# Optimization experiments

Hardware: AMD Instinct MI355X
Metric: run time of the kernel (lower is better)

Reference implementation:

```python
import jax, jax.numpy as jnp
import numpy as np

DIM = 33  # hardcoded in the torch module


def setup_inputs() -> dict:
    key = jax.random.key(0)
    k1, k2, k3 = jax.random.split(key, 3)
    B, H, W = 8, 512, 512
    inp = jax.random.uniform(k1, (B, 3, H, W), dtype=jnp.float32)
    out = jax.random.uniform(k2, (B, 3, H, W), dtype=jnp.float32)
    mask = (jax.random.uniform(k3, (B, 1, H, W)) > 0.5).astype(jnp.float32)
    return {"mask": mask, "input": inp, "output": out}


def _tridistribute(mask, inp, out, dim=DIM):
    # Trilinear scatter-accumulate of `out` pixel colors into a per-image
    # 3D LUT indexed by `inp` pixel colors, masked, then count-normalized.
    B = inp.shape[0]
    binsize = 1.000001 / (dim - 1)
    x = inp / binsize                              # [B,3,H,W]
    idx = jnp.floor(x).astype(jnp.int32)           # lower bin ids, in [0, dim-2]
    frac = x - jnp.floor(x)                        # trilinear fractions
    r_id, g_id, b_id = idx[:, 0], idx[:, 1], idx[:, 2]
    rd = frac[:, 0].reshape(B, -1)                 # [B,N], N = H*W
    gd = frac[:, 1].reshape(B, -1)
    bd = frac[:, 2].reshape(B, -1)
    base = (r_id + g_id * dim + b_id * dim * dim).reshape(B, -1)  # flat corner 000
    m = (mask[:, 0] > 0).astype(inp.dtype).reshape(B, -1)
    ws, offs = [], []
    for db in (0, 1):
        for dg in (0, 1):
            for dr in (0, 1):
                w = ((rd if dr else 1 - rd) * (gd if dg else 1 - gd) * (bd if db else 1 - bd))
                ws.append(w * m)
                offs.append(dr + dg * dim + db * dim * dim)
    w_all = jnp.stack(ws, 0)                                        # [8,B,N]
    idx_all = base[None] + jnp.asarray(offs, jnp.int32)[:, None, None]  # [8,B,N]
    idx_flat = idx_all.transpose(1, 0, 2).reshape(B, -1)            # [B,8N]
    w_flat = w_all.transpose(1, 0, 2).reshape(B, -1)                # [B,8N]
    out_f = out.reshape(B, 3, -1)                                   # [B,3,N]
    vals = (w_all[:, :, None, :] * out_f[None]).transpose(1, 2, 0, 3).reshape(B, 3, -1)  # [B,3,8N]
    nbins = dim ** 3
    # scatter-add per batch element (vmap over B, then over 3 channels)
    lut = jax.vmap(lambda i, v: jax.vmap(lambda vc: jnp.zeros(nbins, inp.dtype).at[i].add(vc))(v))(idx_flat, vals)  # [B,3,nbins]
    cnt1 = jax.vmap(lambda i, w: jnp.zeros(nbins, inp.dtype).at[i].add(w))(idx_flat, w_flat)  # [B,nbins]
    cnt = jnp.broadcast_to(cnt1[:, None, :], lut.shape)             # same count for all 3 channels
    denom = jnp.where(cnt > 0, cnt, 1.0)
    lut = jnp.where(cnt > 0, lut / denom, 0.0)                      # tridistribute.divide
    shape5 = (B, 3, dim, dim, dim)
    return lut.reshape(shape5), cnt.reshape(shape5)


def reference(mask, input, output):
    lut, lut_count = _tridistribute(mask, input, output)
    return lut, lut_count, output
```

## Files before the change

### kernel.cpp

```cpp
#include <hip/hip_runtime.h>
#include <hip/hip_fp16.h>

#define DIM   33
#define NB    (DIM * DIM * DIM)
#define BATCH 8
#define HW    (512 * 512)
#define SLICE (DIM * DIM)
#define NK1   32
#define CAP1  4416
#define W1    256
#define SPAN1 1024
#define SUB2  4
#define NKEY  1024
#define CAP2  192
#define MAXC2 1120

#define G1_OFF 0
#define G2_OFF 256
#define NCNT   (G2_OFF + BATCH * NKEY)
#define A1     8448
#define S1     (BATCH * NK1 * CAP1)
#define A2     (A1 + 3 * S1)
#define S2     (BATCH * NKEY * CAP2)
#define WS_WORDS (A2 + 3 * S2)

static __device__ __forceinline__ unsigned f2h(float x) {
    return (unsigned)__half_as_ushort(__float2half(x));
}
static __device__ __forceinline__ float h2f(unsigned u) {
    return __half2float(__ushort_as_half((unsigned short)(u & 0xffffu)));
}
static __device__ __forceinline__ unsigned pack2(float a, float b) {
    return f2h(a) | (f2h(b) << 16);
}

__global__ __launch_bounds__(256) void zero_counters(int* __restrict__ ws)
{
    int i = blockIdx.x * 256 + threadIdx.x;
    if (i < NCNT) ws[i] = 0;
}

__global__ __launch_bounds__(256) void sort1(const float* __restrict__ mask,
                                             const float* __restrict__ inp,
                                             const float* __restrict__ outp,
                                             int* __restrict__ ws,
                                             float* __restrict__ outcopy)
{
    __shared__ int hist[NK1], basev[NK1], startL[NK1];
    __shared__ unsigned       stX[SPAN1];
    __shared__ unsigned       stY[SPAN1];
    __shared__ unsigned       o01[SPAN1];
    __shared__ unsigned short o2h[SPAN1];
    __shared__ unsigned short rnk[SPAN1];
    __shared__ unsigned short sidx[SPAN1];

    const int bid = blockIdx.x;
    const int w   = bid & (W1 - 1);
    const int b   = bid >> 8;

    if (threadIdx.x < NK1) hist[threadIdx.x] = 0;
    __syncthreads();

    const float binsize = 1.000001f / 32.0f;
    const size_t off = (size_t)w * SPAN1;
    const float* mk  = mask + (size_t)b * HW + off;
    const float* inR = inp  + (size_t)b * 3 * HW + off;
    const float* inG = inR + HW;
    const float* inB = inR + 2 * HW;
    const float* oR  = outp + (size_t)b * 3 * HW + off;
    const float* oG  = oR + HW;
    const float* oB  = oR + 2 * HW;
    float* cR = outcopy + (size_t)b * 3 * HW + off;
    float* cG = cR + HW;
    float* cB = cR + 2 * HW;

    const int o = threadIdx.x * 4;

    {
        float4 mv = *(const float4*)(mk + o);
        float4 rv = *(const float4*)(inR + o);
        float4 gv = *(const float4*)(inG + o);
        float4 bv = *(const float4*)(inB + o);
        float4 a0 = *(const float4*)(oR + o);
        float4 a1 = *(const float4*)(oG + o);
        float4 a2 = *(const float4*)(oB + o);

        *(float4*)(cR + o) = a0;
        *(float4*)(cG + o) = a1;
        *(float4*)(cB + o) = a2;

        float mm[4] = {mv.x, mv.y, mv.z, mv.w};
        float rr[4] = {rv.x, rv.y, rv.z, rv.w};
        float gg[4] = {gv.x, gv.y, gv.z, gv.w};
        float bb[4] = {bv.x, bv.y, bv.z, bv.w};
        float q0[4] = {a0.x, a0.y, a0.z, a0.w};
        float q1[4] = {a1.x, a1.y, a1.z, a1.w};
        float q2[4] = {a2.x, a2.y, a2.z, a2.w};
        #pragma unroll
        for (int r = 0; r < 4; ++r) {
            o01[o + r] = pack2(q0[r], q1[r]);
            o2h[o + r] = (unsigned short)f2h(q2[r]);
            unsigned sx = 0, sy = 0;
            if (mm[r] > 0.0f) {
                float xr = rr[r] / binsize;
                float xg = gg[r] / binsize;
                float xb = bb[r] / binsize;
                float fr = floorf(xr), fg = floorf(xg), fb = floorf(xb);
                int ir = (int)fr, ig = (int)fg, ib = (int)fb;
                int rd12 = (int)((xr - fr) * 4095.0f + 0.5f);
                int gd12 = (int)((xg - fg) * 4095.0f + 0.5f);
                int bd12 = (int)((xb - fb) * 4095.0f + 0.5f);
                sx = (unsigned)ir | ((unsigned)ig << 5) | ((unsigned)rd12 << 10)
                   | ((unsigned)(gd12 & 0x3FF) << 22);
                sy = (unsigned)(gd12 >> 10) | ((unsigned)bd12 << 2)
                   | ((unsigned)ib << 14) | (1u << 19);
                rnk[o + r] = (unsigned short)atomicAdd(&hist[ib], 1);
            }
            stX[o + r] = sx;
            stY[o + r] = sy;
        }
    }
    __syncthreads();

    if (threadIdx.x < NK1) {
        int c = hist[threadIdx.x];
        basev[threadIdx.x] = c ? atomicAdd(&ws[G1_OFF + b * NK1 + threadIdx.x], c) : 0;
        int v = c;
        #pragma unroll
        for (int d = 1; d < 32; d <<= 1) {
            int t = __shfl_up(v, d);
            if (threadIdx.x >= d) v += t;
        }
        startL[threadIdx.x] = v - c;
    }
    __syncthreads();

    {
        #pragma unroll
        for (int r = 0; r < 4; ++r) {
            unsigned sy = stY[o + r];
            if (sy >> 19) {
                int k = (sy >> 14) & 31;
                sidx[startL[k] + rnk[o + r]] = (unsigned short)(o + r);
            }
        }
    }
    __syncthreads();

    const int nlive = startL[NK1 - 1] + hist[NK1 - 1];
    unsigned* x1 = (unsigned*)(ws + A1);
    unsigned* y1 = x1 + S1;
    unsigned* z1 = x1 + 2 * S1;
    for (int j = threadIdx.x; j < nlive; j += 256) {
        int t = sidx[j];
        unsigned sy = stY[t];
        int k = (sy >> 14) & 31;
        int gs = basev[k] + (j - startL[k]);
        if (gs < CAP1) {
            size_t base = (size_t)(b * NK1 + k) * CAP1 + gs;
            x1[base] = stX[t];
            y1[base] = (sy & 0x3FFFu) | ((o01[t] & 0xFFFFu) << 14);
            z1[base] = (o01[t] >> 16) | ((unsigned)o2h[t] << 16);
        }
    }
}

__global__ __launch_bounds__(256) void sort2(int* __restrict__ ws)
{
    __shared__ unsigned       xL[MAXC2], yL[MAXC2], zL[MAXC2];
    __shared__ unsigned short rnkL[MAXC2], sidxL[MAXC2];
    __shared__ int hist[32], basev[32], startL[32];

    const int bid = blockIdx.x;
    const int s   = bid & (SUB2 - 1);
    const int ib  = (bid >> 2) & 31;
    const int b   = bid >> 7;

    if (threadIdx.x < 32) hist[threadIdx.x] = 0;
    __syncthreads();

    int n1 = ws[G1_OFF + b * NK1 + ib];
    if (n1 > CAP1) n1 = CAP1;
    const int beg = n1 * s / SUB2;
    const int end = n1 * (s + 1) / SUB2;
    const int cntn = end - beg;

    const unsigned* x1 = (const unsigned*)(ws + A1);
    const unsigned* y1 = x1 + S1;
    const unsigned* z1 = x1 + 2 * S1;
    const size_t base1 = (size_t)(b * NK1 + ib) * CAP1 + beg;

    for (int i = threadIdx.x; i < cntn; i += 256) {
        unsigned x = x1[base1 + i];
        xL[i] = x;
        yL[i] = y1[base1 + i];
        zL[i] = z1[base1 + i];
        rnkL[i] = (unsigned short)atomicAdd(&hist[(x >> 5) & 31], 1);
    }
    __syncthreads();

    if (threadIdx.x < 32) {
        int c = hist[threadIdx.x];
        basev[threadIdx.x] = c
            ? atomicAdd(&ws[G2_OFF + ((b << 10) | (threadIdx.x << 5) | ib)], c) : 0;
        int v = c;
        #pragma unroll
        for (int d = 1; d < 32; d <<= 1) {
            int t = __shfl_up(v, d);
            if (threadIdx.x >= d) v += t;
        }
        startL[threadIdx.x] = v - c;
    }
    __syncthreads();

    for (int i = threadIdx.x; i < cntn; i += 256) {
        int k = (xL[i] >> 5) & 31;
        sidxL[startL[k] + rnkL[i]] = (unsigned short)i;
    }
    __syncthreads();

    unsigned* x2 = (unsigned*)(ws + A2);
    unsigned* y2 = x2 + S2;
    unsigned* z2 = x2 + 2 * S2;
    for (int j = threadIdx.x; j < cntn; j += 256) {
        int t = sidxL[j];
        unsigned x = xL[t];
        int k = (x >> 5) & 31;
        int gs = basev[k] + (j - startL[k]);
        if (gs < CAP2) {
            size_t b2 = (size_t)((b << 10) | (k << 5) | ib) * CAP2 + gs;
            x2[b2] = x;
            y2[b2] = yL[t];
            z2[b2] = zL[t];
        }
    }
}

__global__ __launch_bounds__(256) void gather_pass(const int* __restrict__ ws,
                                                   float* __restrict__ lut,
                                                   float* __restrict__ cnt)
{
    __shared__ float4 vL[4][CAP2];
    __shared__ float  rdL[4][CAP2];
    __shared__ int    histL[4][32];
    __shared__ int    startL[4][32];
    __shared__ float  partL[4][64][4];

    const int bid   = blockIdx.x;
    const int b     = bid / SLICE;
    const int rem   = bid % SLICE;
    const int gOut  = rem / DIM;
    const int blOut = rem % DIM;

    const int wv    = threadIdx.x >> 6;
    const int lane  = threadIdx.x & 63;
    const int ghalf = (wv >> 1) & 1;
    const int bhalf = wv & 1;
    const int ig    = gOut - 1 + ghalf;
    const int ib    = blOut - 1 + bhalf;
    const bool valid = ((unsigned)ig < 32u) && ((unsigned)ib < 32u);

    if (lane < 32) histL[wv][lane] = 0;
    __syncthreads();

    const unsigned* x2 = (const unsigned*)(ws + A2);
    const unsigned* y2 = x2 + S2;
    const unsigned* z2 = x2 + 2 * S2;

    const float inv = 1.0f / 4095.0f;
    int n = 0;
    int    ranks[3] = {0, 0, 0};
    int    irs[3]   = {0, 0, 0};
    float4 vreg[3];
    float  rdreg[3] = {0.f, 0.f, 0.f};
    if (valid) {
        int key = (ig << 5) | ib;
        n = ws[G2_OFF + ((b << 10) | key)];
        if (n > CAP2) n = CAP2;
        size_t kb = (size_t)((b << 10) | key) * CAP2;
        #pragma unroll
        for (int t = 0; t < 3; ++t) {
            int i = lane + t * 64;
            if (i < n) {
                unsigned x = x2[kb + i];
                unsigned y = y2[kb + i];
                unsigned z = z2[kb + i];
                float rd = (float)((x >> 10) & 0xFFF) * inv;
                float gd = (float)(((x >> 22) & 0x3FF) | ((y & 3u) << 10)) * inv;
                float bd = (float)((y >> 2) & 0xFFF) * inv;
                float o0 = h2f(y >> 14);
                float o1 = h2f(z);
                float o2 = h2f(z >> 16);
                float wg_ = ghalf ? (1.0f - gd) : gd;
                float wb_ = bhalf ? (1.0f - bd) : bd;
                float wgb = wg_ * wb_;
                vreg[t]  = make_float4(wgb * o0, wgb * o1, wgb * o2, wgb);
                rdreg[t] = rd;
                irs[t]   = x & 31;
                ranks[t] = atomicAdd(&histL[wv][irs[t]], 1);
            }
        }
    }
    __syncthreads();

    {
        int h = (lane < 32) ? histL[wv][lane] : 0;
        int v = h;
        #pragma unroll
        for (int o = 1; o < 32; o <<= 1) {
            int t = __shfl_up(v, o, 32);
            if ((lane & 31) >= o) v += t;
        }
        if (lane < 32) startL[wv][lane] = v - h;
    }
    __syncthreads();

    if (valid) {
        #pragma unroll
        for (int t = 0; t < 3; ++t) {
            int i = lane + t * 64;
            if (i < n) {
                int pos = startL[wv][irs[t]] + ranks[t];
                vL[wv][pos]  = vreg[t];
                rdL[wv][pos] = rdreg[t];
            }
        }
    }
    __syncthreads();

    float4 acc = make_float4(0.f, 0.f, 0.f, 0.f);
    if (valid) {
        const int run = lane >> 1;
        const int kk  = lane & 1;
        int s = startL[wv][run];
        int e = s + histL[wv][run];
        for (int j = s; j < e; ++j) {
            float4 v = vL[wv][j];
            float rd = rdL[wv][j];
            float wr_ = kk ? (1.0f - rd) : rd;
            acc.x += wr_ * v.x;
            acc.y += wr_ * v.y;
            acc.z += wr_ * v.z;
            acc.w += wr_ * v.w;
        }
    }
    *(float4*)partL[wv][lane] = acc;
    __syncthreads();

    if (threadIdx.x < DIM * 4) {
        int r  = threadIdx.x >> 2;
        int ch = threadIdx.x & 3;
        float v = 0.f, c = 0.f;
        #pragma unroll
        for (int w2 = 0; w2 < 4; ++w2) {
            if (r < 32) {
                v += partL[w2][2 * r + 1][ch == 3 ? 3 : ch];
                c += partL[w2][2 * r + 1][3];
            }
            if (r > 0) {
                v += partL[w2][2 * r - 2][ch == 3 ? 3 : ch];
                c += partL[w2][2 * r - 2][3];
            }
        }
        int bin = r + gOut * DIM + blOut * SLICE;
        size_t ob = (size_t)b * 3 * NB;
        if (ch == 3) {
            cnt[ob + bin]          = c;
            cnt[ob + NB + bin]     = c;
            cnt[ob + 2 * NB + bin] = c;
        } else {
            lut[ob + (size_t)ch * NB + bin] = (c > 0.0f) ? v / c : 0.0f;
        }
    }
}

__global__ void tridist_scatter(const float* __restrict__ mask,
                                const float* __restrict__ inp,
                                const float* __restrict__ outp,
                                float* __restrict__ lut,
                                float* __restrict__ cnt)
{
    int i = blockIdx.x * blockDim.x + threadIdx.x;
    if (i >= BATCH * HW) return;
    int b = i / HW;
    int p = i - b * HW;

    float m = mask[(size_t)b * HW + p];
    if (!(m > 0.0f)) return;

    const float binsize = 1.000001f / 32.0f;
    size_t ibase = (size_t)b * 3 * HW + p;
    float xr = inp[ibase] / binsize;
    float xg = inp[ibase + HW] / binsize;
    float xb = inp[ibase + 2 * HW] / binsize;
    float flr = floorf(xr), flg = floorf(xg), flb = floorf(xb);
    int ir = (int)flr, ig = (int)flg, ib = (int)flb;
    float rd = xr - flr, gd = xg - flg, bd = xb - flb;
    int base = ir + ig * DIM + ib * DIM * DIM;
    float o0 = outp[ibase], o1 = outp[ibase + HW], o2 = outp[ibase + 2 * HW];
    float wr[2] = {1.0f - rd, rd};
    float wg_[2] = {1.0f - gd, gd};
    float wb[2] = {1.0f - bd, bd};
    float* lut0 = lut + (size_t)b * 3 * NB;
    float* cnt0 = cnt + (size_t)b * 3 * NB;
    #pragma unroll
    for (int db = 0; db < 2; ++db)
        #pragma unroll
        for (int dg = 0; dg < 2; ++dg)
            #pragma unroll
            for (int dr = 0; dr < 2; ++dr) {
                float wv2 = (wr[dr] * wg_[dg]) * wb[db];
                int bin = base + dr + dg * DIM + db * DIM * DIM;
                atomicAdd(cnt0 + bin, wv2);
                atomicAdd(lut0 + bin, wv2 * o0);
                atomicAdd(lut0 + NB + bin, wv2 * o1);
                atomicAdd(lut0 + 2 * NB + bin, wv2 * o2);
            }
}

__global__ void tridist_finalize(float* __restrict__ lut, float* __restrict__ cnt)
{
    int i = blockIdx.x * blockDim.x + threadIdx.x;
    if (i >= BATCH * NB) return;
    int b = i / NB;
    int j = i - b * NB;
    float c = cnt[(size_t)b * 3 * NB + j];
    bool nz = (c > 0.0f);
    #pragma unroll
    for (int ch = 0; ch < 3; ++ch) {
        size_t off = ((size_t)b * 3 + ch) * NB + j;
        float v = lut[off];
        lut[off] = nz ? (v / c) : 0.0f;
        cnt[off] = c;
    }
}

__global__ void copy_out(const float4* __restrict__ src,
                         float4* __restrict__ dst, int n4)
{
    int i = blockIdx.x * blockDim.x + threadIdx.x;
    int stride = gridDim.x * blockDim.x;
    for (; i < n4; i += stride) dst[i] = src[i];
}

extern "C" void kernel_launch(void* const* d_in, const int* in_sizes, int n_in,
                              void* d_out, int out_size, void* d_ws, size_t ws_size,
                              hipStream_t stream)
{
    const float* mask = (const float*)d_in[0];
    const float* inp  = (const float*)d_in[1];
    const float* outp = (const float*)d_in[2];

    float* out     = (float*)d_out;
    float* lut     = out;
    float* cnt     = out + (size_t)BATCH * 3 * NB;
    float* outcopy = out + (size_t)2 * BATCH * 3 * NB;

    size_t need = (size_t)WS_WORDS * sizeof(int);

    if (ws_size >= need) {
        int* ws = (int*)d_ws;
        zero_counters<<<(NCNT + 255) / 256, 256, 0, stream>>>(ws);
        sort1<<<BATCH * W1, 256, 0, stream>>>(mask, inp, outp, ws, outcopy);
        sort2<<<BATCH * NK1 * SUB2, 256, 0, stream>>>(ws);
        gather_pass<<<BATCH * SLICE, 256, 0, stream>>>(ws, lut, cnt);
    } else {
        hipMemsetAsync(out, 0, (size_t)2 * BATCH * 3 * NB * sizeof(float), stream);
        tridist_scatter<<<(BATCH * HW + 255) / 256, 256, 0, stream>>>(mask, inp, outp, lut, cnt);
        tridist_finalize<<<(BATCH * NB + 255) / 256, 256, 0, stream>>>(lut, cnt);
        int n4 = BATCH * 3 * HW / 4;
        copy_out<<<2048, 256, 0, stream>>>((const float4*)outp, (float4*)outcopy, n4);
    }
}
```

Baseline: 63.01 us.

## Sort by joint g/r key in sort2 and pass run tables to gather

sort2 now builds a 1024-bin joint histogram over (g-bin, r-bin), so each bucket it writes out is already ordered by r within each of its four sub-chunks. It also writes a per-key run-offset table (absRun) into the workspace. gather_pass reads these offsets directly and drops its shared-memory histogram, atomics, scan and scatter, along with two of its barriers. In exchange, sort2 does a larger 1024-entry scan, extra table writes and extra global reads in gather, and each lane now loops over four segments instead of one.

```diff
diff --git a/kernel.cpp b/kernel.cpp
--- a/kernel.cpp
+++ b/kernel.cpp
@@ -22,7 +22,9 @@
 #define S1     (BATCH * NK1 * CAP1)
 #define A2     (A1 + 3 * S1)
 #define S2     (BATCH * NKEY * CAP2)
-#define WS_WORDS (A2 + 3 * S2)
+#define RT_OFF (A2 + 3 * S2)
+#define RT_ENT (BATCH * NKEY * SUB2 * 33)
+#define WS_WORDS (RT_OFF + (RT_ENT + 1) / 2)
 
 static __device__ __forceinline__ unsigned f2h(float x) {
     return (unsigned)__half_as_ushort(__float2half(x));
@@ -165,18 +167,24 @@
     }
 }
 
-__global__ __launch_bounds__(256) void sort2(int* __restrict__ ws)
+__global__ __launch_bounds__(256) void sort2(int* __restrict__ ws,
+                                             unsigned short* __restrict__ absRun)
 {
     __shared__ unsigned       xL[MAXC2], yL[MAXC2], zL[MAXC2];
     __shared__ unsigned short rnkL[MAXC2], sidxL[MAXC2];
-    __shared__ int hist[32], basev[32], startL[32];
+    __shared__ int hist[1024];
+    __shared__ int startL[1024];
+    __shared__ int basev[32];
+    __shared__ int wsum[4];
 
     const int bid = blockIdx.x;
     const int s   = bid & (SUB2 - 1);
     const int ib  = (bid >> 2) & 31;
     const int b   = bid >> 7;
-
-    if (threadIdx.x < 32) hist[threadIdx.x] = 0;
+    const int tid = threadIdx.x;
+
+    #pragma unroll
+    for (int k = 0; k < 4; ++k) hist[tid + k * 256] = 0;
     __syncthreads();
 
     int n1 = ws[G1_OFF + b * NK1 + ib];
@@ -190,60 +198,93 @@
     const unsigned* z1 = x1 + 2 * S1;
     const size_t base1 = (size_t)(b * NK1 + ib) * CAP1 + beg;
 
-    for (int i = threadIdx.x; i < cntn; i += 256) {
+    for (int i = tid; i < cntn; i += 256) {
         unsigned x = x1[base1 + i];
         xL[i] = x;
         yL[i] = y1[base1 + i];
         zL[i] = z1[base1 + i];
-        rnkL[i] = (unsigned short)atomicAdd(&hist[(x >> 5) & 31], 1);
-    }
-    __syncthreads();
-
-    if (threadIdx.x < 32) {
-        int c = hist[threadIdx.x];
-        basev[threadIdx.x] = c
-            ? atomicAdd(&ws[G2_OFF + ((b << 10) | (threadIdx.x << 5) | ib)], c) : 0;
-        int v = c;
-        #pragma unroll
-        for (int d = 1; d < 32; d <<= 1) {
+        int joint = (((x >> 5) & 31) << 5) | (x & 31);
+        rnkL[i] = (unsigned short)atomicAdd(&hist[joint], 1);
+    }
+    __syncthreads();
+
+    int sums[4];
+    int local = 0;
+    {
+        const int b4 = tid * 4;
+        #pragma unroll
+        for (int k = 0; k < 4; ++k) { sums[k] = local; local += hist[b4 + k]; }
+        int lane = tid & 63, wid = tid >> 6;
+        int v = local;
+        #pragma unroll
+        for (int d = 1; d < 64; d <<= 1) {
             int t = __shfl_up(v, d);
-            if (threadIdx.x >= d) v += t;
-        }
-        startL[threadIdx.x] = v - c;
-    }
-    __syncthreads();
-
-    for (int i = threadIdx.x; i < cntn; i += 256) {
-        int k = (xL[i] >> 5) & 31;
-        sidxL[startL[k] + rnkL[i]] = (unsigned short)i;
+            if (lane >= d) v += t;
+        }
+        if (lane == 63) wsum[wid] = v;
+        __syncthreads();
+        if (tid == 0) {
+            int a = 0;
+            #pragma unroll
+            for (int w2 = 0; w2 < 4; ++w2) { int t = wsum[w2]; wsum[w2] = a; a += t; }
+        }
+        __syncthreads();
+        int excl = v - local + wsum[wid];
+        const int b4b = tid * 4;
+        #pragma unroll
+        for (int k = 0; k < 4; ++k) startL[b4b + k] = excl + sums[k];
+    }
+    __syncthreads();
+
+    if (tid < 32) {
+        int keyStart = startL[tid << 5];
+        int keyEnd   = (tid == 31) ? cntn : startL[(tid + 1) << 5];
+        int c = keyEnd - keyStart;
+        basev[tid] = c
+            ? atomicAdd(&ws[G2_OFF + ((b << 10) | (tid << 5) | ib)], c) : 0;
+    }
+    __syncthreads();
+
+    for (int i = tid; i < cntn; i += 256) {
+        unsigned x = xL[i];
+        int joint = (((x >> 5) & 31) << 5) | (x & 31);
+        sidxL[startL[joint] + rnkL[i]] = (unsigned short)i;
+    }
+    for (int e = tid; e < 32 * 33; e += 256) {
+        int ig = e / 33, r = e - ig * 33;
+        int keyStart = startL[ig << 5];
+        int keyEnd   = (ig == 31) ? cntn : startL[(ig + 1) << 5];
+        int rel = (r == 32) ? (keyEnd - keyStart)
+                            : (startL[(ig << 5) + r] - keyStart);
+        size_t idx = ((size_t)((b << 10) | (ig << 5) | ib) * SUB2 + s) * 33 + r;
+        absRun[idx] = (unsigned short)(basev[ig] + rel);
     }
     __syncthreads();
 
     unsigned* x2 = (unsigned*)(ws + A2);
     unsigned* y2 = x2 + S2;
     unsigned* z2 = x2 + 2 * S2;
-    for (int j = threadIdx.x; j < cntn; j += 256) {
+    for (int j = tid; j < cntn; j += 256) {
         int t = sidxL[j];
         unsigned x = xL[t];
-        int k = (x >> 5) & 31;
-        int gs = basev[k] + (j - startL[k]);
+        int ig = (x >> 5) & 31;
+        int gs = basev[ig] + (j - startL[ig << 5]);
         if (gs < CAP2) {
-            size_t b2 = (size_t)((b << 10) | (k << 5) | ib) * CAP2 + gs;
-            x2[b2] = x;
-            y2[b2] = yL[t];
-            z2[b2] = zL[t];
+            size_t d = (size_t)((b << 10) | (ig << 5) | ib) * CAP2 + gs;
+            x2[d] = x;
+            y2[d] = yL[t];
+            z2[d] = zL[t];
         }
     }
 }
 
 __global__ __launch_bounds__(256) void gather_pass(const int* __restrict__ ws,
+                                                   const unsigned short* __restrict__ absRun,
                                                    float* __restrict__ lut,
                                                    float* __restrict__ cnt)
 {
     __shared__ float4 vL[4][CAP2];
     __shared__ float  rdL[4][CAP2];
-    __shared__ int    histL[4][32];
-    __shared__ int    startL[4][32];
     __shared__ float  partL[4][64][4];
 
     const int bid   = blockIdx.x;
@@ -260,24 +301,30 @@
     const int ib    = blOut - 1 + bhalf;
     const bool valid = ((unsigned)ig < 32u) && ((unsigned)ib < 32u);
 
-    if (lane < 32) histL[wv][lane] = 0;
-    __syncthreads();
-
     const unsigned* x2 = (const unsigned*)(ws + A2);
     const unsigned* y2 = x2 + S2;
     const unsigned* z2 = x2 + 2 * S2;
 
     const float inv = 1.0f / 4095.0f;
     int n = 0;
-    int    ranks[3] = {0, 0, 0};
-    int    irs[3]   = {0, 0, 0};
-    float4 vreg[3];
-    float  rdreg[3] = {0.f, 0.f, 0.f};
+    int s4[SUB2], e4[SUB2];
     if (valid) {
-        int key = (ig << 5) | ib;
-        n = ws[G2_OFF + ((b << 10) | key)];
+        int gkey = (b << 10) | (ig << 5) | ib;
+        n = ws[G2_OFF + gkey];
         if (n > CAP2) n = CAP2;
-        size_t kb = (size_t)((b << 10) | key) * CAP2;
+
+        const int run = lane >> 1;
+        size_t rbase = (size_t)gkey * SUB2 * 33;
+        #pragma unroll
+        for (int q = 0; q < SUB2; ++q) {
+            int ss = absRun[rbase + q * 33 + run];
+            int ee = absRun[rbase + q * 33 + run + 1];
+            if (ss > n) ss = n;
+            if (ee > n) ee = n;
+            s4[q] = ss; e4[q] = ee;
+        }
+
+        size_t kb = (size_t)gkey * CAP2;
         #pragma unroll
         for (int t = 0; t < 3; ++t) {
             int i = lane + t * 64;
@@ -294,35 +341,8 @@
                 float wg_ = ghalf ? (1.0f - gd) : gd;
                 float wb_ = bhalf ? (1.0f - bd) : bd;
                 float wgb = wg_ * wb_;
-                vreg[t]  = make_float4(wgb * o0, wgb * o1, wgb * o2, wgb);
-                rdreg[t] = rd;
-                irs[t]   = x & 31;
-                ranks[t] = atomicAdd(&histL[wv][irs[t]], 1);
-            }
-        }
-    }
-    __syncthreads();
-
-    {
-        int h = (lane < 32) ? histL[wv][lane] : 0;
-        int v = h;
-        #pragma unroll
-        for (int o = 1; o < 32; o <<= 1) {
-            int t = __shfl_up(v, o, 32);
-            if ((lane & 31) >= o) v += t;
-        }
-        if (lane < 32) startL[wv][lane] = v - h;
-    }
-    __syncthreads();
-
-    if (valid) {
-        #pragma unroll
-        for (int t = 0; t < 3; ++t) {
-            int i = lane + t * 64;
-            if (i < n) {
-                int pos = startL[wv][irs[t]] + ranks[t];
-                vL[wv][pos]  = vreg[t];
-                rdL[wv][pos] = rdreg[t];
+                vL[wv][i]  = make_float4(wgb * o0, wgb * o1, wgb * o2, wgb);
+                rdL[wv][i] = rd;
             }
         }
     }
@@ -330,18 +350,18 @@
 
     float4 acc = make_float4(0.f, 0.f, 0.f, 0.f);
     if (valid) {
-        const int run = lane >> 1;
-        const int kk  = lane & 1;
-        int s = startL[wv][run];
-        int e = s + histL[wv][run];
-        for (int j = s; j < e; ++j) {
-            float4 v = vL[wv][j];
-            float rd = rdL[wv][j];
-            float wr_ = kk ? (1.0f - rd) : rd;
-            acc.x += wr_ * v.x;
-            acc.y += wr_ * v.y;
-            acc.z += wr_ * v.z;
-            acc.w += wr_ * v.w;
+        const int kk = lane & 1;
+        #pragma unroll
+        for (int q = 0; q < SUB2; ++q) {
+            for (int j = s4[q]; j < e4[q]; ++j) {
+                float4 v = vL[wv][j];
+                float rd = rdL[wv][j];
+                float wr_ = kk ? (1.0f - rd) : rd;
+                acc.x += wr_ * v.x;
+                acc.y += wr_ * v.y;
+                acc.z += wr_ * v.z;
+                acc.w += wr_ * v.w;
+            }
         }
     }
     *(float4*)partL[wv][lane] = acc;
@@ -460,10 +480,12 @@
 
     if (ws_size >= need) {
         int* ws = (int*)d_ws;
+        unsigned short* absRun = (unsigned short*)((int*)d_ws + RT_OFF);
+
         zero_counters<<<(NCNT + 255) / 256, 256, 0, stream>>>(ws);
         sort1<<<BATCH * W1, 256, 0, stream>>>(mask, inp, outp, ws, outcopy);
-        sort2<<<BATCH * NK1 * SUB2, 256, 0, stream>>>(ws);
-        gather_pass<<<BATCH * SLICE, 256, 0, stream>>>(ws, lut, cnt);
+        sort2<<<BATCH * NK1 * SUB2, 256, 0, stream>>>(ws, absRun);
+        gather_pass<<<BATCH * SLICE, 256, 0, stream>>>(ws, absRun, lut, cnt);
     } else {
         hipMemsetAsync(out, 0, (size_t)2 * BATCH * 3 * NB * sizeof(float), stream);
         tridist_scatter<<<(BATCH * HW + 255) / 256, 256, 0, stream>>>(mask, inp, outp, lut, cnt);
```

Result: no change. 63.29 us (+0.4%).
